# Kernel tuning notes

Hardware: AMD Instinct MI355X
Metric: run time of the kernel (lower is better)

The kernel has to match this reference:

```python
import jax, jax.numpy as jnp
import numpy as np

N = 100000   # nodes
E = 600000   # edges (before self loops)
D = 128      # dim_latent = H*F
H = 4        # heads
F = 32       # out_feats per head
L = 3        # num GATConv layers (conv_0 + 2)


def setup_inputs() -> dict:
    key = jax.random.key(0)
    ks = jax.random.split(key, 10)
    return {
        "weights": jax.random.normal(ks[0], (N,), jnp.float32),
        "lin_W": jax.random.normal(ks[1], (D, 1), jnp.float32) * 0.1,
        "lin_b": jnp.zeros((D,), jnp.float32),
        "fc_W": jax.random.normal(ks[2], (L, D, D), jnp.float32) * (1.0 / np.sqrt(D)),
        "attn_l": jax.random.normal(ks[3], (L, H, F), jnp.float32) * 0.1,
        "attn_r": jax.random.normal(ks[4], (L, H, F), jnp.float32) * 0.1,
        "conv_b": jnp.zeros((L, D), jnp.float32),
        "pred_W": jax.random.normal(ks[5], (1, D), jnp.float32) * 0.1,
        "pred_b": jnp.zeros((1,), jnp.float32),
        "src": jax.random.randint(ks[6], (E,), 0, N, jnp.int32),
        "dst": jax.random.randint(ks[7], (E,), 0, N, jnp.int32),
    }


def _leaky(x, slope):
    return jnp.where(x >= 0, x, slope * x)


def _gat_conv(x, fc_W, attn_l, attn_r, bias, src, dst):
    # DGL GATConv: bias-free fc, per-head additive attention, edge softmax over dst
    h = (x @ fc_W.T).reshape(N, H, F)                      # [N,H,F]
    el = jnp.sum(h * attn_l[None], axis=-1)                # [N,H]
    er = jnp.sum(h * attn_r[None], axis=-1)                # [N,H]
    e = _leaky(el[src] + er[dst], 0.2)                     # [Etot,H]
    m = jax.ops.segment_max(e, dst, num_segments=N)        # [N,H]
    a = jnp.exp(e - m[dst])                                # [Etot,H]
    s = jax.ops.segment_sum(a, dst, num_segments=N)        # [N,H]
    alpha = a / s[dst]                                     # [Etot,H]
    msg = h[src] * alpha[:, :, None]                       # [Etot,H,F]
    out = jax.ops.segment_sum(msg, dst, num_segments=N)    # [N,H,F]
    out = out + bias.reshape(H, F)[None]
    return out.reshape(N, H * F)


def reference(weights, lin_W, lin_b, fc_W, attn_l, attn_r, conv_b, pred_W, pred_b, src, dst):
    # add self loops (dgl.add_self_loop)
    loop = jnp.arange(N, dtype=src.dtype)
    s_full = jnp.concatenate([src, loop])
    d_full = jnp.concatenate([dst, loop])

    x = weights[:, None] @ lin_W.T + lin_b                 # [N,D]
    for i in range(L):
        if i > 0:
            x = _leaky(x, 0.01)                            # nn.LeakyReLU default
        x = _gat_conv(x, fc_W[i], attn_l[i], attn_r[i], conv_b[i], s_full, d_full)
    logits = x @ pred_W.T + pred_b                         # [N,1]
    return logits
```

## Files before the change

### kernel.cpp

```cpp
#include <hip/hip_runtime.h>
#include <hip/hip_bf16.h>
#include <math.h>


__device__ __forceinline__ float leaky02(float x) {
    return x >= 0.f ? x : 0.2f * x;
}
__device__ __forceinline__ float leaky01(float x) {
    return x >= 0.f ? x : 0.01f * x;
}

__device__ __forceinline__ unsigned short f2bf(float f) {
    unsigned u = __float_as_uint(f);
    unsigned r = u + 0x7FFFu + ((u >> 16) & 1u);
    return (unsigned short)(r >> 16);
}
__device__ __forceinline__ float bf2f(unsigned short s) {
    return __uint_as_float(((unsigned)s) << 16);
}

typedef __attribute__((ext_vector_type(8))) short bf16x8;
typedef __attribute__((ext_vector_type(8))) unsigned short u16x8;
typedef __attribute__((ext_vector_type(4))) float f32x4;

__global__ __launch_bounds__(1024) void prep_kernel(
    int* __restrict__ deg, int N,
    const float* __restrict__ fc_W, const float* __restrict__ attn_l,
    const float* __restrict__ attn_r,
    short* __restrict__ Wh, short* __restrict__ Wl,
    short* __restrict__ Mh, short* __restrict__ Ml,
    const float* __restrict__ lW, const float* __restrict__ lb,
    const float* __restrict__ cb2, const float* __restrict__ pW,
    const float* __restrict__ pb,
    float* __restrict__ c1, float* __restrict__ c2, float* __restrict__ prm)
{
    const int nbi = (N + 1023) >> 10;
    const int b = blockIdx.x;
    const int t = threadIdx.x;

    if (b < nbi) {
        int i = b * 1024 + t;
        if (i < N) deg[i] = 1;
        if (i < 2 * 16384) {
            const float* W = fc_W + 16384;
            int l    = i >> 14;
            int p    = i & 16383;
            int j    = p & 7;
            int lane = (p >> 3) & 63;
            int c    = (p >> 9) & 7;
            int kk   = p >> 12;
            int mr   = lane & 15;
            int quad = lane >> 4;
            int row  = c * 16 + mr;
            int d    = kk * 32 + quad * 8 + j;
            float f = W[(size_t)l * 16384 + row * 128 + d];
            unsigned short hi = f2bf(f);
            Wh[i] = (short)hi;
            Wl[i] = (short)f2bf(f - bf2f(hi));
        }
    } else if (b < nbi + 2) {
        int l = b - nbi;
        const float* W  = fc_W + (size_t)(l + 1) * 16384;
        const float* al = attn_l + (l + 1) * 128;
        const float* ar = attn_r + (l + 1) * 128;
        short* mh = Mh + (size_t)l * 16 * 128;
        short* ml = Ml + (size_t)l * 16 * 128;
        int r = t >> 7;
        int d = t & 127;
        int hh = r & 3;
        const float* av = (r < 4) ? al : ar;
        float s = 0.f;
#pragma unroll
        for (int f = 0; f < 32; ++f)
            s += W[(size_t)(hh * 32 + f) * 128 + d] * av[hh * 32 + f];
        unsigned short hi = f2bf(s);
        mh[r * 128 + d] = (short)hi;
        ml[r * 128 + d] = (short)f2bf(s - bf2f(hi));
        mh[(r + 8) * 128 + d] = 0;
        ml[(r + 8) * 128 + d] = 0;
    } else {
        __shared__ float sh1[128], sh2[128], sh3[128], sh4[128], sh5[128];
        const float* W0 = fc_W;
        const float* al = attn_l;
        const float* ar = attn_r;
        int j = t >> 3, sub = t & 7;
        float s1 = 0.f, s2 = 0.f;
        int d0 = sub * 16;
#pragma unroll
        for (int k = 0; k < 16; ++k) {
            float wv = W0[j * 128 + d0 + k];
            s1 += lW[d0 + k] * wv;
            s2 += lb[d0 + k] * wv;
        }
#pragma unroll
        for (int m = 1; m <= 4; m <<= 1) {
            s1 += __shfl_xor(s1, m, 64);
            s2 += __shfl_xor(s2, m, 64);
        }
        if (sub == 0) {
            c1[j] = s1; c2[j] = s2;
            sh1[j] = s1 * al[j]; sh2[j] = s2 * al[j];
            sh3[j] = s1 * ar[j]; sh4[j] = s2 * ar[j];
            sh5[j] = cb2[j] * pW[j];
        }
        __syncthreads();
        if (t < 4) {
            float p = 0.f, q = 0.f, r = 0.f, s = 0.f;
            for (int f = 0; f < 32; ++f) {
                p += sh1[t * 32 + f]; q += sh2[t * 32 + f];
                r += sh3[t * 32 + f]; s += sh4[t * 32 + f];
            }
            prm[t] = p; prm[4 + t] = q; prm[8 + t] = r; prm[12 + t] = s;
        }
        if (t == 0) {
            float cs = 0.f;
            for (int k = 0; k < 128; ++k) cs += sh5[k];
            prm[16] = cs + pb[0];
        }
    }
}

__global__ __launch_bounds__(256) void deg_count_slot_kernel(
    const int* __restrict__ dst, int* __restrict__ deg,
    int* __restrict__ slot, int E)
{
    int i = blockIdx.x * 256 + threadIdx.x;
    if (i < E) slot[i] = atomicAdd(&deg[dst[i]], 1);
}

#define SCAN_TILE 1024

__global__ __launch_bounds__(256) void scanA_kernel(
    const int* __restrict__ deg, int* __restrict__ bsum, int N)
{
    __shared__ int ws[4];
    int b = blockIdx.x, t = threadIdx.x;
    int base = b * SCAN_TILE + t * 4;
    int s = 0;
#pragma unroll
    for (int k = 0; k < 4; ++k) {
        int i = base + k;
        if (i < N) s += deg[i];
    }
#pragma unroll
    for (int m = 32; m >= 1; m >>= 1) s += __shfl_xor(s, m, 64);
    if ((t & 63) == 0) ws[t >> 6] = s;
    __syncthreads();
    if (t == 0) bsum[b] = ws[0] + ws[1] + ws[2] + ws[3];
}

__global__ __launch_bounds__(1024) void scanB_kernel(
    int* __restrict__ bsum, int* __restrict__ bpre, int* __restrict__ rowp,
    int NB, int N)
{
    __shared__ int sh[1024];
    int t = threadIdx.x;
    int v = (t < NB) ? bsum[t] : 0;
    sh[t] = v;
    __syncthreads();
    for (int off = 1; off < 1024; off <<= 1) {
        int u = (t >= off) ? sh[t - off] : 0;
        __syncthreads();
        sh[t] += u;
        __syncthreads();
    }
    if (t < NB) bpre[t] = sh[t] - v;
    if (t == 1023) rowp[N] = sh[1023];
}

__global__ __launch_bounds__(256) void scanC_kernel(
    const int* __restrict__ deg, const int* __restrict__ bpre,
    int* __restrict__ rowp, int* __restrict__ col, int N)
{
    __shared__ int sh[256];
    int b = blockIdx.x, t = threadIdx.x;
    int base = b * SCAN_TILE + t * 4;
    int v[4];
#pragma unroll
    for (int k = 0; k < 4; ++k) {
        int i = base + k;
        v[k] = (i < N) ? deg[i] : 0;
    }
    int tsum = v[0] + v[1] + v[2] + v[3];
    sh[t] = tsum;
    __syncthreads();
    for (int off = 1; off < 256; off <<= 1) {
        int u = (t >= off) ? sh[t - off] : 0;
        __syncthreads();
        sh[t] += u;
        __syncthreads();
    }
    int pre = bpre[b] + sh[t] - tsum;
#pragma unroll
    for (int k = 0; k < 4; ++k) {
        int i = base + k;
        if (i < N) {
            rowp[i] = pre;
            col[pre] = i;
        }
        pre += v[k];
    }
}

__global__ __launch_bounds__(256) void scatter2_kernel(
    const int* __restrict__ src, const int* __restrict__ dst,
    const int* __restrict__ slot, const int* __restrict__ rowp,
    int* __restrict__ col, int E)
{
    int i = blockIdx.x * 256 + threadIdx.x;
    if (i < E) col[rowp[dst[i]] + slot[i]] = src[i];
}

__global__ __launch_bounds__(256) void agg0_kernel(
    const float* __restrict__ w, const float* __restrict__ c1,
    const float* __restrict__ c2, const float* __restrict__ prm,
    const int* __restrict__ rowp, const int* __restrict__ col,
    const float* __restrict__ bias, unsigned short* __restrict__ xout, int N)
{
    const int lane = threadIdx.x & 63;
    const int q    = lane >> 4;
    const int l16  = lane & 15;
    const int v    = blockIdx.x * 16 + (threadIdx.x >> 6) * 4 + q;
    if (v >= N) return;

    const int r0 = rowp[v], r1 = rowp[v + 1];
    const int head = l16 >> 2;
    const int e4   = l16 & 3;
    const int f0   = l16 * 8;
    const float pl = prm[head],     ql = prm[4 + head];
    const float pr = prm[8 + head], qr = prm[12 + head];

    const float wv  = w[v];
    const float erq = wv * pr + qr;
    const float mref = leaky02(wv * pl + ql + erq);

    float S = 0.f, Sw = 0.f;
    for (int j = r0 + e4; j < r1; j += 4) {
        int u = col[j];
        float wu = w[u];
        float e = leaky02(wu * pl + ql + erq);
        float d = fminf(e - mref, 80.f);
        float p = __expf(d);
        S += p; Sw += p * wu;
    }
    S  += __shfl_xor(S, 1, 64);  S  += __shfl_xor(S, 2, 64);
    Sw += __shfl_xor(Sw, 1, 64); Sw += __shfl_xor(Sw, 2, 64);
    const float t = Sw / S;

    float4 a0 = *reinterpret_cast<const float4*>(&c1[f0]);
    float4 a1 = *reinterpret_cast<const float4*>(&c1[f0 + 4]);
    float4 g0 = *reinterpret_cast<const float4*>(&c2[f0]);
    float4 g1 = *reinterpret_cast<const float4*>(&c2[f0 + 4]);
    float4 b0 = *reinterpret_cast<const float4*>(&bias[f0]);
    float4 b1 = *reinterpret_cast<const float4*>(&bias[f0 + 4]);
    const float aa[8] = {a0.x, a0.y, a0.z, a0.w, a1.x, a1.y, a1.z, a1.w};
    const float gg[8] = {g0.x, g0.y, g0.z, g0.w, g1.x, g1.y, g1.z, g1.w};
    const float bb[8] = {b0.x, b0.y, b0.z, b0.w, b1.x, b1.y, b1.z, b1.w};

    u16x8 o;
#pragma unroll
    for (int k = 0; k < 8; ++k)
        o[k] = f2bf(leaky01(t * aa[k] + gg[k] + bb[k]));
    *reinterpret_cast<u16x8*>(&xout[(size_t)v * 128 + f0]) = o;
}

__global__ __launch_bounds__(256) void gemm_mfma_kernel(
    const unsigned short* __restrict__ xb, const short* __restrict__ Wh,
    const short* __restrict__ Wl, const short* __restrict__ Mh,
    const short* __restrict__ Ml, unsigned short* __restrict__ hb,
    float* __restrict__ el, float* __restrict__ er,
    const float* __restrict__ pW, float* __restrict__ yel,
    int N, int mode)
{
    const int lane = threadIdx.x & 63;
    const int wv   = threadIdx.x >> 6;
    const int m0   = blockIdx.x * 128 + wv * 32;
    const int mr   = lane & 15;
    const int quad = lane >> 4;

    int r0 = m0 + mr;      if (r0 > N - 1) r0 = N - 1;
    int r1 = m0 + 16 + mr; if (r1 > N - 1) r1 = N - 1;
    const unsigned short* xp0 = xb + (size_t)r0 * 128 + quad * 8;
    const unsigned short* xp1 = xb + (size_t)r1 * 128 + quad * 8;

    f32x4 acc0[8], acc1[8], acce0, acce1;
#pragma unroll
    for (int c = 0; c < 8; ++c) {
        acc0[c] = (f32x4){0.f, 0.f, 0.f, 0.f};
        acc1[c] = (f32x4){0.f, 0.f, 0.f, 0.f};
    }
    acce0 = (f32x4){0.f, 0.f, 0.f, 0.f};
    acce1 = (f32x4){0.f, 0.f, 0.f, 0.f};

#pragma unroll
    for (int kk = 0; kk < 4; ++kk) {
        bf16x8 a0 = *reinterpret_cast<const bf16x8*>(xp0 + kk * 32);
        bf16x8 a1 = *reinterpret_cast<const bf16x8*>(xp1 + kk * 32);

        const int kb = kk * 32 + quad * 8;
        bf16x8 bh[8], bl[8];
#pragma unroll
        for (int c = 0; c < 8; ++c) {
            const size_t wo = (size_t)((kk * 8 + c) * 64 + lane) * 8;
            bh[c] = *reinterpret_cast<const bf16x8*>(Wh + wo);
            bl[c] = *reinterpret_cast<const bf16x8*>(Wl + wo);
        }
        bf16x8 eh = *reinterpret_cast<const bf16x8*>(Mh + (size_t)mr * 128 + kb);
        bf16x8 eo = *reinterpret_cast<const bf16x8*>(Ml + (size_t)mr * 128 + kb);
#pragma unroll
        for (int c = 0; c < 8; ++c) {
            acc0[c] = __builtin_amdgcn_mfma_f32_16x16x32_bf16(a0, bh[c], acc0[c], 0, 0, 0);
            acc0[c] = __builtin_amdgcn_mfma_f32_16x16x32_bf16(a0, bl[c], acc0[c], 0, 0, 0);
            acc1[c] = __builtin_amdgcn_mfma_f32_16x16x32_bf16(a1, bh[c], acc1[c], 0, 0, 0);
            acc1[c] = __builtin_amdgcn_mfma_f32_16x16x32_bf16(a1, bl[c], acc1[c], 0, 0, 0);
        }
        acce0 = __builtin_amdgcn_mfma_f32_16x16x32_bf16(a0, eh, acce0, 0, 0, 0);
        acce0 = __builtin_amdgcn_mfma_f32_16x16x32_bf16(a0, eo, acce0, 0, 0, 0);
        acce1 = __builtin_amdgcn_mfma_f32_16x16x32_bf16(a1, eh, acce1, 0, 0, 0);
        acce1 = __builtin_amdgcn_mfma_f32_16x16x32_bf16(a1, eo, acce1, 0, 0, 0);
    }

    if (mode == 0) {
#pragma unroll
        for (int i = 0; i < 4; ++i) {
            int rowA = m0 + quad * 4 + i;
            if (rowA < N) {
                unsigned short* hp = hb + (size_t)rowA * 128 + mr;
#pragma unroll
                for (int c = 0; c < 8; ++c) hp[c * 16] = f2bf(acc0[c][i]);
                if (mr < 4)       el[(size_t)rowA * 4 + mr]       = acce0[i];
                else if (mr < 8)  er[(size_t)rowA * 4 + (mr - 4)] = acce0[i];
            }
            int rowB = m0 + 16 + quad * 4 + i;
            if (rowB < N) {
                unsigned short* hp = hb + (size_t)rowB * 128 + mr;
#pragma unroll
                for (int c = 0; c < 8; ++c) hp[c * 16] = f2bf(acc1[c][i]);
                if (mr < 4)       el[(size_t)rowB * 4 + mr]       = acce1[i];
                else if (mr < 8)  er[(size_t)rowB * 4 + (mr - 4)] = acce1[i];
            }
        }
    } else {
        float pw[8];
#pragma unroll
        for (int c = 0; c < 8; ++c) pw[c] = pW[mr + c * 16];
#pragma unroll
        for (int i = 0; i < 4; ++i) {
            int rowA = m0 + quad * 4 + i;
            {
                float y[4];
#pragma unroll
                for (int h = 0; h < 4; ++h)
                    y[h] = acc0[2 * h][i] * pw[2 * h] + acc0[2 * h + 1][i] * pw[2 * h + 1];
#pragma unroll
                for (int d = 1; d < 16; d <<= 1) {
#pragma unroll
                    for (int h = 0; h < 4; ++h) y[h] += __shfl_xor(y[h], d, 64);
                }
                if (rowA < N) {
                    if (mr < 4) {
                        float2 o; o.x = y[mr]; o.y = acce0[i];
                        *reinterpret_cast<float2*>(&yel[(size_t)rowA * 8 + mr * 2]) = o;
                    } else if (mr < 8) {
                        er[(size_t)rowA * 4 + (mr - 4)] = acce0[i];
                    }
                }
            }
            int rowB = m0 + 16 + quad * 4 + i;
            {
                float y[4];
#pragma unroll
                for (int h = 0; h < 4; ++h)
                    y[h] = acc1[2 * h][i] * pw[2 * h] + acc1[2 * h + 1][i] * pw[2 * h + 1];
#pragma unroll
                for (int d = 1; d < 16; d <<= 1) {
#pragma unroll
                    for (int h = 0; h < 4; ++h) y[h] += __shfl_xor(y[h], d, 64);
                }
                if (rowB < N) {
                    if (mr < 4) {
                        float2 o; o.x = y[mr]; o.y = acce1[i];
                        *reinterpret_cast<float2*>(&yel[(size_t)rowB * 8 + mr * 2]) = o;
                    } else if (mr < 8) {
                        er[(size_t)rowB * 4 + (mr - 4)] = acce1[i];
                    }
                }
            }
        }
    }
}

__global__ __launch_bounds__(256) void agg_mid_kernel(
    const unsigned short* __restrict__ hb, const float* __restrict__ el,
    const float* __restrict__ er, const int* __restrict__ rowp,
    const int* __restrict__ col, const float* __restrict__ bias,
    unsigned short* __restrict__ xout, int N)
{
    const int lane = threadIdx.x & 63;
    const int q    = lane >> 4;
    const int l16  = lane & 15;
    const int v    = blockIdx.x * 16 + (threadIdx.x >> 6) * 4 + q;
    if (v >= N) return;

    const int r0 = rowp[v], r1 = rowp[v + 1];
    const int head = l16 >> 2;
    const int f0   = l16 * 8;
    const float erq = er[(size_t)v * 4 + head];
    const float el_self = el[(size_t)v * 4 + head];
    const float mref = leaky02(el_self + erq);

    float s = 0.f;
    float acc[8];
#pragma unroll
    for (int k = 0; k < 8; ++k) acc[k] = 0.f;

    float elA = el_self;
    u16x8 hvA = *reinterpret_cast<const u16x8*>(&hb[(size_t)v * 128 + f0]);
    int jB = (r0 + 1 < r1) ? r0 + 1 : r1 - 1;
    int uB = col[jB];
    float elB = el[(size_t)uB * 4 + head];
    u16x8 hvB = *reinterpret_cast<const u16x8*>(&hb[(size_t)uB * 128 + f0]);

    for (int j = r0; j < r1; j += 2) {
        int jA2 = (j + 2 < r1) ? j + 2 : r1 - 1;
        int uA2 = col[jA2];
        float elA2 = el[(size_t)uA2 * 4 + head];
        u16x8 hvA2 = *reinterpret_cast<const u16x8*>(&hb[(size_t)uA2 * 128 + f0]);

        {
            float e = leaky02(elA + erq);
            float d = fminf(e - mref, 80.f);
            float p = __expf(d);
            s += p;
#pragma unroll
            for (int k = 0; k < 8; ++k) acc[k] += p * bf2f(hvA[k]);
        }

        if (j + 1 < r1) {
            int jB2 = (j + 3 < r1) ? j + 3 : r1 - 1;
            int uB2 = col[jB2];
            float elB2 = el[(size_t)uB2 * 4 + head];
            u16x8 hvB2 = *reinterpret_cast<const u16x8*>(&hb[(size_t)uB2 * 128 + f0]);

            float e = leaky02(elB + erq);
            float d = fminf(e - mref, 80.f);
            float p = __expf(d);
            s += p;
#pragma unroll
            for (int k = 0; k < 8; ++k) acc[k] += p * bf2f(hvB[k]);

            elB = elB2; hvB = hvB2;
        }
        elA = elA2; hvA = hvA2;
    }
    const float is = 1.f / s;

    float4 b0 = *reinterpret_cast<const float4*>(&bias[f0]);
    float4 b1 = *reinterpret_cast<const float4*>(&bias[f0 + 4]);
    const float bb[8] = {b0.x, b0.y, b0.z, b0.w, b1.x, b1.y, b1.z, b1.w};

    u16x8 o;
#pragma unroll
    for (int k = 0; k < 8; ++k) o[k] = f2bf(leaky01(acc[k] * is + bb[k]));
    *reinterpret_cast<u16x8*>(&xout[(size_t)v * 128 + f0]) = o;
}

__global__ __launch_bounds__(256) void agg2_kernel(
    const float* __restrict__ yel, const float* __restrict__ er,
    const int* __restrict__ rowp, const int* __restrict__ col,
    const float* __restrict__ prm, float* __restrict__ logits, int N)
{
    const int lane = threadIdx.x & 63;
    const int q    = lane >> 4;
    const int l16  = lane & 15;
    const int v    = blockIdx.x * 16 + (threadIdx.x >> 6) * 4 + q;
    if (v >= N) return;

    const int r0 = rowp[v], r1 = rowp[v + 1];
    const int head = l16 >> 2;
    const int e4   = l16 & 3;
    const float erq = er[(size_t)v * 4 + head];

    float2 selfy = *reinterpret_cast<const float2*>(&yel[(size_t)v * 8 + head * 2]);
    const float mref = leaky02(selfy.y + erq);

    float S = 0.f, A = 0.f;
    for (int j = r0 + e4; j < r1; j += 4) {
        int u = col[j];
        float2 c = *reinterpret_cast<const float2*>(&yel[(size_t)u * 8 + head * 2]);
        float e = leaky02(c.y + erq);
        float d = fminf(e - mref, 80.f);
        float p = __expf(d);
        S += p; A += p * c.x;
    }
    S += __shfl_xor(S, 1, 64); S += __shfl_xor(S, 2, 64);
    A += __shfl_xor(A, 1, 64); A += __shfl_xor(A, 2, 64);
    float part = A / S;
    part += __shfl_xor(part, 4, 64);
    part += __shfl_xor(part, 8, 64);
    if (l16 == 0) logits[v] = part + prm[16];
}

extern "C" void kernel_launch(void* const* d_in, const int* in_sizes, int n_in,
                              void* d_out, int out_size, void* d_ws, size_t ws_size,
                              hipStream_t stream)
{
    const float* weights = (const float*)d_in[0];
    const float* lin_W   = (const float*)d_in[1];
    const float* lin_b   = (const float*)d_in[2];
    const float* fc_W    = (const float*)d_in[3];
    const float* attn_l  = (const float*)d_in[4];
    const float* attn_r  = (const float*)d_in[5];
    const float* conv_b  = (const float*)d_in[6];
    const float* pred_W  = (const float*)d_in[7];
    const float* pred_b  = (const float*)d_in[8];
    const int*   src     = (const int*)d_in[9];
    const int*   dst     = (const int*)d_in[10];

    const int N = in_sizes[0];
    const int E = in_sizes[9];
    const int NB = (N + SCAN_TILE - 1) / SCAN_TILE;
    const int NBI = (N + 1023) / 1024;

    unsigned short* xb = (unsigned short*)d_ws;
    unsigned short* hb = xb + (size_t)N * 128;
    float* el  = (float*)(hb + (size_t)N * 128);
    float* er  = el + (size_t)N * 4;
    float* yel = er + (size_t)N * 4;
    float* c1  = yel + (size_t)N * 8;
    float* c2  = c1 + 128;
    float* prm = c2 + 128;
    short* Whs = (short*)(prm + 32);
    short* Wls = Whs + 2 * 16384;
    short* Mhs = Wls + 2 * 16384;
    short* Mls = Mhs + 2 * 2048;
    int*   deg  = (int*)(Mls + 2 * 2048);
    int*   rowp = deg + N;
    int*   slot = rowp + (N + 1);
    int*   col  = slot + E;
    int*   bsum = col + (E + N);
    int*   bpre = bsum + NB;

    prep_kernel<<<NBI + 3, 1024, 0, stream>>>(
        deg, N, fc_W, attn_l, attn_r, Whs, Wls, Mhs, Mls,
        lin_W, lin_b, conv_b + 2 * 128, pred_W, pred_b, c1, c2, prm);

    deg_count_slot_kernel<<<(E + 255) / 256, 256, 0, stream>>>(dst, deg, slot, E);
    scanA_kernel<<<NB, 256, 0, stream>>>(deg, bsum, N);
    scanB_kernel<<<1, 1024, 0, stream>>>(bsum, bpre, rowp, NB, N);
    scanC_kernel<<<NB, 256, 0, stream>>>(deg, bpre, rowp, col, N);
    scatter2_kernel<<<(E + 255) / 256, 256, 0, stream>>>(src, dst, slot, rowp, col, E);

    agg0_kernel<<<(N + 15) / 16, 256, 0, stream>>>(
        weights, c1, c2, prm, rowp, col, conv_b, xb, N);

    gemm_mfma_kernel<<<(N + 127) / 128, 256, 0, stream>>>(
        xb, Whs, Wls, Mhs, Mls, hb, el, er, pred_W, yel, N, 0);
    agg_mid_kernel<<<(N + 15) / 16, 256, 0, stream>>>(
        hb, el, er, rowp, col, conv_b + 128, xb, N);

    gemm_mfma_kernel<<<(N + 127) / 128, 256, 0, stream>>>(
        xb, Whs + 16384, Wls + 16384, Mhs + 2048, Mls + 2048,
        hb, el, er, pred_W, yel, N, 1);
    agg2_kernel<<<(N + 15) / 16, 256, 0, stream>>>(
        yel, er, rowp, col, prm, (float*)d_out, N);
}
```

Measured before the change: 251.8 us.

## Fuse CSR build kernels into one persistent kernel with grid barriers

Result: slower. 307.8 us (+22.2%).

```diff
diff --git a/kernel.cpp b/kernel.cpp
--- a/kernel.cpp
+++ b/kernel.cpp
@@ -23,7 +23,34 @@
 typedef __attribute__((ext_vector_type(8))) unsigned short u16x8;
 typedef __attribute__((ext_vector_type(4))) float f32x4;
 
-__global__ __launch_bounds__(1024) void prep_kernel(
+__device__ unsigned g_bar_count = 0;
+__device__ unsigned g_bar_gen   = 0;
+
+__device__ __forceinline__ void grid_barrier() {
+    __syncthreads();
+    if (threadIdx.x == 0) {
+        __threadfence();
+        unsigned gen = __hip_atomic_load(&g_bar_gen, __ATOMIC_RELAXED,
+                                         __HIP_MEMORY_SCOPE_AGENT);
+        unsigned arrived = __hip_atomic_fetch_add(&g_bar_count, 1u,
+                                                  __ATOMIC_ACQ_REL,
+                                                  __HIP_MEMORY_SCOPE_AGENT);
+        if (arrived == gridDim.x - 1) {
+            __hip_atomic_store(&g_bar_count, 0u, __ATOMIC_RELAXED,
+                               __HIP_MEMORY_SCOPE_AGENT);
+            __hip_atomic_fetch_add(&g_bar_gen, 1u, __ATOMIC_RELEASE,
+                                   __HIP_MEMORY_SCOPE_AGENT);
+        } else {
+            while (__hip_atomic_load(&g_bar_gen, __ATOMIC_ACQUIRE,
+                                     __HIP_MEMORY_SCOPE_AGENT) == gen)
+                __builtin_amdgcn_s_sleep(1);
+        }
+        __threadfence();
+    }
+    __syncthreads();
+}
+
+__global__ __launch_bounds__(1024) void csr_prep_kernel(
     int* __restrict__ deg, int N,
     const float* __restrict__ fc_W, const float* __restrict__ attn_l,
     const float* __restrict__ attn_r,
@@ -32,54 +59,61 @@
     const float* __restrict__ lW, const float* __restrict__ lb,
     const float* __restrict__ cb2, const float* __restrict__ pW,
     const float* __restrict__ pb,
-    float* __restrict__ c1, float* __restrict__ c2, float* __restrict__ prm)
+    float* __restrict__ c1, float* __restrict__ c2, float* __restrict__ prm,
+    const int* __restrict__ src, const int* __restrict__ dst,
+    int* __restrict__ slot, int E,
+    int* __restrict__ bsum, int* __restrict__ bpre,
+    int* __restrict__ rowp, int* __restrict__ col)
 {
-    const int nbi = (N + 1023) >> 10;
+    __shared__ int   sh_i[1024];
+    __shared__ float sh_f[5 * 128];
+
     const int b = blockIdx.x;
     const int t = threadIdx.x;
-
-    if (b < nbi) {
-        int i = b * 1024 + t;
-        if (i < N) deg[i] = 1;
-        if (i < 2 * 16384) {
-            const float* W = fc_W + 16384;
-            int l    = i >> 14;
-            int p    = i & 16383;
-            int j    = p & 7;
-            int lane = (p >> 3) & 63;
-            int c    = (p >> 9) & 7;
-            int kk   = p >> 12;
-            int mr   = lane & 15;
-            int quad = lane >> 4;
-            int row  = c * 16 + mr;
-            int d    = kk * 32 + quad * 8 + j;
-            float f = W[(size_t)l * 16384 + row * 128 + d];
-            unsigned short hi = f2bf(f);
-            Wh[i] = (short)hi;
-            Wl[i] = (short)f2bf(f - bf2f(hi));
-        }
-    } else if (b < nbi + 2) {
-        int l = b - nbi;
-        const float* W  = fc_W + (size_t)(l + 1) * 16384;
-        const float* al = attn_l + (l + 1) * 128;
-        const float* ar = attn_r + (l + 1) * 128;
-        short* mh = Mh + (size_t)l * 16 * 128;
-        short* ml = Ml + (size_t)l * 16 * 128;
+    const int stride = gridDim.x * 1024;
+
+    for (int i = b * 1024 + t; i < N; i += stride) deg[i] = 1;
+    for (int i = b * 1024 + t; i < 2 * 16384; i += stride) {
+        const float* W = fc_W + 16384;
+        int l    = i >> 14;
+        int p    = i & 16383;
+        int j    = p & 7;
+        int lane = (p >> 3) & 63;
+        int c    = (p >> 9) & 7;
+        int kk   = p >> 12;
+        int mr   = lane & 15;
+        int quad = lane >> 4;
+        int row  = c * 16 + mr;
+        int d    = kk * 32 + quad * 8 + j;
+        float f = W[(size_t)l * 16384 + row * 128 + d];
+        unsigned short hi = f2bf(f);
+        Wh[i] = (short)hi;
+        Wl[i] = (short)f2bf(f - bf2f(hi));
+    }
+    if (b == 1) {
         int r = t >> 7;
         int d = t & 127;
         int hh = r & 3;
-        const float* av = (r < 4) ? al : ar;
-        float s = 0.f;
-#pragma unroll
-        for (int f = 0; f < 32; ++f)
-            s += W[(size_t)(hh * 32 + f) * 128 + d] * av[hh * 32 + f];
-        unsigned short hi = f2bf(s);
-        mh[r * 128 + d] = (short)hi;
-        ml[r * 128 + d] = (short)f2bf(s - bf2f(hi));
-        mh[(r + 8) * 128 + d] = 0;
-        ml[(r + 8) * 128 + d] = 0;
-    } else {
-        __shared__ float sh1[128], sh2[128], sh3[128], sh4[128], sh5[128];
+#pragma unroll
+        for (int l = 0; l < 2; ++l) {
+            const float* W  = fc_W + (size_t)(l + 1) * 16384;
+            const float* al = attn_l + (l + 1) * 128;
+            const float* ar = attn_r + (l + 1) * 128;
+            short* mh = Mh + (size_t)l * 16 * 128;
+            short* ml = Ml + (size_t)l * 16 * 128;
+            const float* av = (r < 4) ? al : ar;
+            float s = 0.f;
+#pragma unroll
+            for (int f = 0; f < 32; ++f)
+                s += W[(size_t)(hh * 32 + f) * 128 + d] * av[hh * 32 + f];
+            unsigned short hi = f2bf(s);
+            mh[r * 128 + d] = (short)hi;
+            ml[r * 128 + d] = (short)f2bf(s - bf2f(hi));
+            mh[(r + 8) * 128 + d] = 0;
+            ml[(r + 8) * 128 + d] = 0;
+        }
+    }
+    if (b == 0) {
         const float* W0 = fc_W;
         const float* al = attn_l;
         const float* ar = attn_r;
@@ -99,116 +133,83 @@
         }
         if (sub == 0) {
             c1[j] = s1; c2[j] = s2;
-            sh1[j] = s1 * al[j]; sh2[j] = s2 * al[j];
-            sh3[j] = s1 * ar[j]; sh4[j] = s2 * ar[j];
-            sh5[j] = cb2[j] * pW[j];
+            sh_f[j]       = s1 * al[j]; sh_f[128 + j] = s2 * al[j];
+            sh_f[256 + j] = s1 * ar[j]; sh_f[384 + j] = s2 * ar[j];
+            sh_f[512 + j] = cb2[j] * pW[j];
         }
         __syncthreads();
         if (t < 4) {
             float p = 0.f, q = 0.f, r = 0.f, s = 0.f;
             for (int f = 0; f < 32; ++f) {
-                p += sh1[t * 32 + f]; q += sh2[t * 32 + f];
-                r += sh3[t * 32 + f]; s += sh4[t * 32 + f];
+                p += sh_f[t * 32 + f];       q += sh_f[128 + t * 32 + f];
+                r += sh_f[256 + t * 32 + f]; s += sh_f[384 + t * 32 + f];
             }
             prm[t] = p; prm[4 + t] = q; prm[8 + t] = r; prm[12 + t] = s;
         }
         if (t == 0) {
             float cs = 0.f;
-            for (int k = 0; k < 128; ++k) cs += sh5[k];
+            for (int k = 0; k < 128; ++k) cs += sh_f[512 + k];
             prm[16] = cs + pb[0];
         }
     }
-}
-
-__global__ __launch_bounds__(256) void deg_count_slot_kernel(
-    const int* __restrict__ dst, int* __restrict__ deg,
-    int* __restrict__ slot, int E)
-{
-    int i = blockIdx.x * 256 + threadIdx.x;
-    if (i < E) slot[i] = atomicAdd(&deg[dst[i]], 1);
-}
-
-#define SCAN_TILE 1024
-
-__global__ __launch_bounds__(256) void scanA_kernel(
-    const int* __restrict__ deg, int* __restrict__ bsum, int N)
-{
-    __shared__ int ws[4];
-    int b = blockIdx.x, t = threadIdx.x;
-    int base = b * SCAN_TILE + t * 4;
-    int s = 0;
-#pragma unroll
-    for (int k = 0; k < 4; ++k) {
-        int i = base + k;
-        if (i < N) s += deg[i];
-    }
-#pragma unroll
-    for (int m = 32; m >= 1; m >>= 1) s += __shfl_xor(s, m, 64);
-    if ((t & 63) == 0) ws[t >> 6] = s;
-    __syncthreads();
-    if (t == 0) bsum[b] = ws[0] + ws[1] + ws[2] + ws[3];
-}
-
-__global__ __launch_bounds__(1024) void scanB_kernel(
-    int* __restrict__ bsum, int* __restrict__ bpre, int* __restrict__ rowp,
-    int NB, int N)
-{
-    __shared__ int sh[1024];
-    int t = threadIdx.x;
-    int v = (t < NB) ? bsum[t] : 0;
-    sh[t] = v;
-    __syncthreads();
-    for (int off = 1; off < 1024; off <<= 1) {
-        int u = (t >= off) ? sh[t - off] : 0;
+    grid_barrier();
+
+    for (int e = b * 1024 + t; e < E; e += stride)
+        slot[e] = atomicAdd(&deg[dst[e]], 1);
+    grid_barrier();
+
+    {
+        int i = b * 1024 + t;
+        int val = (i < N) ? deg[i] : 0;
+#pragma unroll
+        for (int m = 32; m >= 1; m >>= 1) val += __shfl_xor(val, m, 64);
+        if ((t & 63) == 0) sh_i[t >> 6] = val;
         __syncthreads();
-        sh[t] += u;
+        if (t == 0) {
+            int s = 0;
+#pragma unroll
+            for (int k = 0; k < 16; ++k) s += sh_i[k];
+            bsum[b] = s;
+        }
+    }
+    grid_barrier();
+
+    if (b == 0) {
+        int vbs = (t < 128 && t < (int)gridDim.x) ? bsum[t] : 0;
+        if (t < 128) sh_i[t] = vbs;
         __syncthreads();
-    }
-    if (t < NB) bpre[t] = sh[t] - v;
-    if (t == 1023) rowp[N] = sh[1023];
-}
-
-__global__ __launch_bounds__(256) void scanC_kernel(
-    const int* __restrict__ deg, const int* __restrict__ bpre,
-    int* __restrict__ rowp, int* __restrict__ col, int N)
-{
-    __shared__ int sh[256];
-    int b = blockIdx.x, t = threadIdx.x;
-    int base = b * SCAN_TILE + t * 4;
-    int v[4];
-#pragma unroll
-    for (int k = 0; k < 4; ++k) {
-        int i = base + k;
-        v[k] = (i < N) ? deg[i] : 0;
-    }
-    int tsum = v[0] + v[1] + v[2] + v[3];
-    sh[t] = tsum;
-    __syncthreads();
-    for (int off = 1; off < 256; off <<= 1) {
-        int u = (t >= off) ? sh[t - off] : 0;
+        for (int off = 1; off < 128; off <<= 1) {
+            int u = (t >= off && t < 128) ? sh_i[t - off] : 0;
+            __syncthreads();
+            if (t < 128) sh_i[t] += u;
+            __syncthreads();
+        }
+        if (t < (int)gridDim.x) bpre[t] = sh_i[t] - vbs;
+        if (t == 0) rowp[N] = sh_i[127];
+    }
+    grid_barrier();
+
+    {
+        int i = b * 1024 + t;
+        int v = (i < N) ? deg[i] : 0;
+        sh_i[t] = v;
         __syncthreads();
-        sh[t] += u;
-        __syncthreads();
-    }
-    int pre = bpre[b] + sh[t] - tsum;
-#pragma unroll
-    for (int k = 0; k < 4; ++k) {
-        int i = base + k;
+        for (int off = 1; off < 1024; off <<= 1) {
+            int u = (t >= off) ? sh_i[t - off] : 0;
+            __syncthreads();
+            sh_i[t] += u;
+            __syncthreads();
+        }
+        int pre = bpre[b] + sh_i[t] - v;
         if (i < N) {
             rowp[i] = pre;
             col[pre] = i;
         }
-        pre += v[k];
-    }
-}
-
-__global__ __launch_bounds__(256) void scatter2_kernel(
-    const int* __restrict__ src, const int* __restrict__ dst,
-    const int* __restrict__ slot, const int* __restrict__ rowp,
-    int* __restrict__ col, int E)
-{
-    int i = blockIdx.x * 256 + threadIdx.x;
-    if (i < E) col[rowp[dst[i]] + slot[i]] = src[i];
+    }
+    grid_barrier();
+
+    for (int e = b * 1024 + t; e < E; e += stride)
+        col[rowp[dst[e]] + slot[e]] = src[e];
 }
 
 __global__ __launch_bounds__(256) void agg0_kernel(
@@ -519,8 +520,7 @@
 
     const int N = in_sizes[0];
     const int E = in_sizes[9];
-    const int NB = (N + SCAN_TILE - 1) / SCAN_TILE;
-    const int NBI = (N + 1023) / 1024;
+    const int NB = (N + 1023) / 1024;
 
     unsigned short* xb = (unsigned short*)d_ws;
     unsigned short* hb = xb + (size_t)N * 128;
@@ -541,15 +541,10 @@
     int*   bsum = col + (E + N);
     int*   bpre = bsum + NB;
 
-    prep_kernel<<<NBI + 3, 1024, 0, stream>>>(
+    csr_prep_kernel<<<NB, 1024, 0, stream>>>(
         deg, N, fc_W, attn_l, attn_r, Whs, Wls, Mhs, Mls,
-        lin_W, lin_b, conv_b + 2 * 128, pred_W, pred_b, c1, c2, prm);
-
-    deg_count_slot_kernel<<<(E + 255) / 256, 256, 0, stream>>>(dst, deg, slot, E);
-    scanA_kernel<<<NB, 256, 0, stream>>>(deg, bsum, N);
-    scanB_kernel<<<1, 1024, 0, stream>>>(bsum, bpre, rowp, NB, N);
-    scanC_kernel<<<NB, 256, 0, stream>>>(deg, bpre, rowp, col, N);
-    scatter2_kernel<<<(E + 255) / 256, 256, 0, stream>>>(src, dst, slot, rowp, col, E);
+        lin_W, lin_b, conv_b + 2 * 128, pred_W, pred_b, c1, c2, prm,
+        src, dst, slot, E, bsum, bpre, rowp, col);
 
     agg0_kernel<<<(N + 15) / 16, 256, 0, stream>>>(
         weights, c1, c2, prm, rowp, col, conv_b, xb, N);
```
